# Performance work log

Measured on AMD Instinct MI355X. Metric: run time of the kernel, lower is better.

Reference implementation:

```python
import jax, jax.numpy as jnp
import numpy as np

NEG = -1e6  # mask fill value used by d2l.sequence_mask


def setup_inputs() -> dict:
    key = jax.random.key(0)
    k1, k2, k3, k4, k5, k6, k7 = jax.random.split(key, 7)
    B, Q, K, DQ, DK, H, DV = 8, 256, 1024, 256, 256, 128, 128
    queries = jax.random.normal(k1, (B, Q, DQ), dtype=jnp.float32)
    keys = jax.random.normal(k2, (B, K, DK), dtype=jnp.float32)
    values = jax.random.normal(k3, (B, K, DV), dtype=jnp.float32)
    valid_lens = jax.random.randint(k4, (B,), 1, K + 1, dtype=jnp.int32)
    # learned params (nn.Linear stores weight as [out, in]; apply as x @ W.T)
    W_q = jax.random.normal(k5, (H, DQ), dtype=jnp.float32) / np.sqrt(DQ)
    W_k = jax.random.normal(k6, (H, DK), dtype=jnp.float32) / np.sqrt(DK)
    w_v = jax.random.normal(k7, (H,), dtype=jnp.float32) / np.sqrt(H)
    return {"queries": queries, "keys": keys, "values": values,
            "valid_lens": valid_lens, "W_q": W_q, "W_k": W_k, "w_v": w_v}


def reference(queries, keys, values, valid_lens, W_q, W_k, w_v):
    # projections
    q = jnp.einsum('bqd,hd->bqh', queries, W_q)   # [B,Q,H]
    k = jnp.einsum('bkd,hd->bkh', keys, W_k)      # [B,K,H]
    # broadcast add + tanh -> [B,Q,K,H] (the fusion-headroom intermediate)
    features = jnp.tanh(q[:, :, None, :] + k[:, None, :, :])
    scores = jnp.einsum('bqkh,h->bqk', features, w_v)  # [B,Q,K]
    # masked softmax: valid_lens is per-batch (dim==1 path)
    klen = scores.shape[-1]
    mask = jnp.arange(klen)[None, None, :] < valid_lens[:, None, None]
    scores = jnp.where(mask, scores, NEG)
    weights = jax.nn.softmax(scores, axis=-1)
    # dropout is identity in eval mode
    return jnp.einsum('bqk,bkv->bqv', weights, values)
```

## Files before the change

### kernel.cpp

```cpp
#include <hip/hip_runtime.h>


#define Bb 8
#define Qn 256
#define Kk 1024
#define Dd 256
#define Hh 128
#define DVv 128

__device__ __forceinline__ float fexp2(float x) { return __builtin_amdgcn_exp2f(x); }
__device__ __forceinline__ float frcp(float x)  { return __builtin_amdgcn_rcpf(x); }

__global__ __launch_bounds__(256)
void repack_w(const float* __restrict__ Wq, const float* __restrict__ Wk,
              float4* __restrict__ Wq4T, float4* __restrict__ Wk4T)
{
    const int blk = blockIdx.x;
    const float* src = (blk < 32) ? Wq : Wk;
    float4*      dst = (blk < 32) ? Wq4T : Wk4T;
    const int idx = (blk & 31) * 256 + threadIdx.x;
    const int g = idx >> 7;
    const int h = idx & 127;
    dst[idx] = *(const float4*)(src + (size_t)h * Dd + g * 4);
}

__global__ __launch_bounds__(512)
void proj_exp_kernel(const float* __restrict__ queries,
                     const float* __restrict__ keys,
                     const float4* __restrict__ Wq4T,
                     const float4* __restrict__ Wk4T,
                     float* __restrict__ EqT,
                     float* __restrict__ EkT)
{
    __shared__ float Xs[16 * 256];
    const int blk = blockIdx.x;
    const float* X; const float4* W4; float* outT; int RB; int i0;
    if (blk < 128) { X = queries; W4 = Wq4T; outT = EqT; RB = Qn; i0 = blk * 16; }
    else           { X = keys;    W4 = Wk4T; outT = EkT; RB = Kk; i0 = (blk - 128) * 16; }
    const int tid = threadIdx.x;
    const int h   = tid & 127;
    const int r4  = __builtin_amdgcn_readfirstlane(tid >> 7);

    {
        const float4* xsrc = (const float4*)(X + (size_t)i0 * Dd);
#pragma unroll
        for (int s = 0; s < 2; ++s) {
            const int idx = tid + 512 * s;
            *(float4*)(Xs + idx * 4) = xsrc[idx];
        }
    }
    __syncthreads();

    float acc[4] = {0.f, 0.f, 0.f, 0.f};
    const float4* wp = W4 + h;
    const float*  xr = Xs + (r4 * 4) * 256;
#pragma unroll 8
    for (int g = 0; g < 64; ++g) {
        const float4 w = wp[(size_t)g * 128];
#pragma unroll
        for (int i = 0; i < 4; ++i) {
            const float4 x = *(const float4*)(xr + i * 256 + g * 4);
            acc[i] = fmaf(x.x, w.x, acc[i]);
            acc[i] = fmaf(x.y, w.y, acc[i]);
            acc[i] = fmaf(x.z, w.z, acc[i]);
            acc[i] = fmaf(x.w, w.w, acc[i]);
        }
    }
    const int b    = i0 / RB;
    const int rloc = (i0 % RB) + r4 * 4;
    float4 o;
    o.x = fexp2(acc[0] * 2.885390082f);
    o.y = fexp2(acc[1] * 2.885390082f);
    o.z = fexp2(acc[2] * 2.885390082f);
    o.w = fexp2(acc[3] * 2.885390082f);
    *(float4*)(outT + (size_t)b * Hh * RB + (size_t)h * RB + rloc) = o;
}

__global__ __launch_bounds__(256)
void score_kernel(const float* __restrict__ EqT,
                  const float* __restrict__ EkT,
                  const float* __restrict__ wv,
                  const int* __restrict__ valid_lens,
                  float* __restrict__ S)
{
    __shared__ float eqs[128 * 8];
    __shared__ float w2s[128];
    const int blk = blockIdx.x;
    const int b   = blk & 7;
    const int rem = blk >> 3;
    const int kt  = rem & 3;
    const int qt  = rem >> 2;
    const int len = valid_lens[b];
    if (kt * 256 >= len) return;

    const int tid = threadIdx.x;
    const int k   = kt * 256 + tid;
    const int q0  = qt * 8;

    {
        const int hh = tid >> 1, part = tid & 1;
        *(float4*)(eqs + hh * 8 + part * 4) =
            *(const float4*)(EqT + (size_t)b * Hh * Qn + (size_t)hh * Qn + q0 + part * 4);
        if (tid < 128) w2s[tid] = -2.0f * wv[tid];
    }
    __syncthreads();

    const float* ekp = EkT + (size_t)b * Hh * Kk + k;
    float a[8];
#pragma unroll
    for (int j = 0; j < 8; ++j) a[j] = 0.f;

#pragma unroll 4
    for (int h = 0; h < Hh; ++h) {
        const float ek = ekp[(size_t)h * Kk];
        const float w2 = w2s[h];
        const float4 e0 = *(const float4*)(eqs + h * 8);
        const float4 e1 = *(const float4*)(eqs + h * 8 + 4);
        a[0] = fmaf(w2, frcp(fmaf(e0.x, ek, 1.0f)), a[0]);
        a[1] = fmaf(w2, frcp(fmaf(e0.y, ek, 1.0f)), a[1]);
        a[2] = fmaf(w2, frcp(fmaf(e0.z, ek, 1.0f)), a[2]);
        a[3] = fmaf(w2, frcp(fmaf(e0.w, ek, 1.0f)), a[3]);
        a[4] = fmaf(w2, frcp(fmaf(e1.x, ek, 1.0f)), a[4]);
        a[5] = fmaf(w2, frcp(fmaf(e1.y, ek, 1.0f)), a[5]);
        a[6] = fmaf(w2, frcp(fmaf(e1.z, ek, 1.0f)), a[6]);
        a[7] = fmaf(w2, frcp(fmaf(e1.w, ek, 1.0f)), a[7]);
    }
    float* srow = S + (size_t)(b * Qn + q0) * Kk + k;
#pragma unroll
    for (int j = 0; j < 8; ++j) srow[(size_t)j * Kk] = a[j];
}

__global__ __launch_bounds__(512)
void softmax_pv_kernel(const float* __restrict__ S,
                       const float* __restrict__ values,
                       const int* __restrict__ valid_lens,
                       float* __restrict__ out)
{
    __shared__ float  s_sc[4][Kk];
    __shared__ float4 s_part[7][4][32];
    __shared__ float  s_inv[4];

    const int blk  = blockIdx.x;
    const int b    = blk & 7;
    const int q0   = (blk >> 3) << 2;
    const int tid  = threadIdx.x;
    const int lane = tid & 63;
    const int wave = __builtin_amdgcn_readfirstlane(tid >> 6);
    const int len  = valid_lens[b];

#pragma unroll
    for (int j = 0; j < 4; ++j) {
        const float* sr = S + (size_t)(b * Qn + q0 + j) * Kk;
        for (int k = tid; k < len; k += 512) s_sc[j][k] = sr[k];
    }
    __syncthreads();

    if (wave < 4) {
        const int q = wave;
        float m = -3.0e38f;
        for (int i = lane; i < len; i += 64) m = fmaxf(m, s_sc[q][i]);
#pragma unroll
        for (int off = 32; off > 0; off >>= 1) m = fmaxf(m, __shfl_xor(m, off));
        float sum = 0.f;
        for (int i = lane; i < len; i += 64) {
            const float p = fexp2((s_sc[q][i] - m) * 1.44269504f);
            s_sc[q][i] = p;
            sum += p;
        }
#pragma unroll
        for (int off = 32; off > 0; off >>= 1) sum += __shfl_xor(sum, off);
        if (lane == 0) s_inv[q] = frcp(sum);
    }
    __syncthreads();

    {
        const int slice = tid >> 5;
        const int l32   = tid & 31;
        const int v4    = l32 << 2;
        const float* vp = values + (size_t)b * Kk * DVv + v4;
        float a[4][4];
#pragma unroll
        for (int q = 0; q < 4; ++q) { a[q][0]=0.f; a[q][1]=0.f; a[q][2]=0.f; a[q][3]=0.f; }
        for (int k = slice; k < len; k += 16) {
            const float4 val = *(const float4*)(vp + (size_t)k * DVv);
            const float w0 = s_sc[0][k], w1 = s_sc[1][k], w2 = s_sc[2][k], w3 = s_sc[3][k];
            a[0][0] = fmaf(w0, val.x, a[0][0]);
            a[0][1] = fmaf(w0, val.y, a[0][1]);
            a[0][2] = fmaf(w0, val.z, a[0][2]);
            a[0][3] = fmaf(w0, val.w, a[0][3]);
            a[1][0] = fmaf(w1, val.x, a[1][0]);
            a[1][1] = fmaf(w1, val.y, a[1][1]);
            a[1][2] = fmaf(w1, val.z, a[1][2]);
            a[1][3] = fmaf(w1, val.w, a[1][3]);
            a[2][0] = fmaf(w2, val.x, a[2][0]);
            a[2][1] = fmaf(w2, val.y, a[2][1]);
            a[2][2] = fmaf(w2, val.z, a[2][2]);
            a[2][3] = fmaf(w2, val.w, a[2][3]);
            a[3][0] = fmaf(w3, val.x, a[3][0]);
            a[3][1] = fmaf(w3, val.y, a[3][1]);
            a[3][2] = fmaf(w3, val.z, a[3][2]);
            a[3][3] = fmaf(w3, val.w, a[3][3]);
        }
#pragma unroll
        for (int q = 0; q < 4; ++q)
#pragma unroll
            for (int x = 0; x < 4; ++x) a[q][x] += __shfl_xor(a[q][x], 32);
        if (wave > 0 && lane < 32) {
#pragma unroll
            for (int q = 0; q < 4; ++q)
                s_part[wave - 1][q][l32] = make_float4(a[q][0], a[q][1], a[q][2], a[q][3]);
        }
        __syncthreads();
        if (wave == 0 && lane < 32) {
#pragma unroll
            for (int q = 0; q < 4; ++q) {
                float r0 = a[q][0], r1 = a[q][1], r2 = a[q][2], r3 = a[q][3];
#pragma unroll
                for (int w = 0; w < 7; ++w) {
                    const float4 p = s_part[w][q][l32];
                    r0 += p.x; r1 += p.y; r2 += p.z; r3 += p.w;
                }
                const float inv = s_inv[q];
                *(float4*)(out + (size_t)(b * Qn + q0 + q) * DVv + v4) =
                    make_float4(r0 * inv, r1 * inv, r2 * inv, r3 * inv);
            }
        }
    }
}

extern "C" void kernel_launch(void* const* d_in, const int* in_sizes, int n_in,
                              void* d_out, int out_size, void* d_ws, size_t ws_size,
                              hipStream_t stream) {
    (void)in_sizes; (void)n_in; (void)out_size; (void)ws_size;
    const float* queries    = (const float*)d_in[0];
    const float* keys       = (const float*)d_in[1];
    const float* values     = (const float*)d_in[2];
    const int*   valid_lens = (const int*)  d_in[3];
    const float* Wq         = (const float*)d_in[4];
    const float* Wk         = (const float*)d_in[5];
    const float* wvv        = (const float*)d_in[6];
    float* out = (float*)d_out;

    float* Wq4T = (float*)d_ws;
    float* Wk4T = Wq4T + (size_t)Dd * Hh;
    float* EqT  = Wk4T + (size_t)Dd * Hh;
    float* EkT  = EqT + (size_t)Bb * Hh * Qn;
    float* S    = EkT + (size_t)Bb * Hh * Kk;

    repack_w       <<<  64, 256, 0, stream>>>(Wq, Wk, (float4*)Wq4T, (float4*)Wk4T);
    proj_exp_kernel<<< 640, 512, 0, stream>>>(queries, keys, (const float4*)Wq4T,
                                              (const float4*)Wk4T, EqT, EkT);
    score_kernel   <<<1024, 256, 0, stream>>>(EqT, EkT, wvv, valid_lens, S);
    softmax_pv_kernel<<<512, 512, 0, stream>>>(S, values, valid_lens, out);
}
```

Measured before the change: 145.0 us.

## Fuse score, softmax and PV into one attention kernel; retile projection through LDS

The score kernel and the softmax/PV kernel are merged into a single attn_kernel. Each block computes scores for two queries directly into LDS, so the global score matrix S is never written or re-read. The fusion uses the identity tanh(x) = 1 - 2/(1+e^{2x}), which turns the softmax max into a min over the rcp sums. The projection kernel is also retiled to 256 threads, staging W and X chunks through LDS with two h-columns per thread. In exchange, the EkT streaming over h is repeated for every query pair (eight queries per block before, two now), and each block does more serial work per query.

```diff
diff --git a/kernel.cpp b/kernel.cpp
--- a/kernel.cpp
+++ b/kernel.cpp
@@ -24,7 +24,7 @@
     dst[idx] = *(const float4*)(src + (size_t)h * Dd + g * 4);
 }
 
-__global__ __launch_bounds__(512)
+__global__ __launch_bounds__(256)
 void proj_exp_kernel(const float* __restrict__ queries,
                      const float* __restrict__ keys,
                      const float4* __restrict__ Wq4T,
@@ -32,139 +32,133 @@
                      float* __restrict__ EqT,
                      float* __restrict__ EkT)
 {
-    __shared__ float Xs[16 * 256];
+    __shared__ float Xs[16 * 64];
+    __shared__ float Ws[4][16 * 128];
+
     const int blk = blockIdx.x;
     const float* X; const float4* W4; float* outT; int RB; int i0;
     if (blk < 128) { X = queries; W4 = Wq4T; outT = EqT; RB = Qn; i0 = blk * 16; }
     else           { X = keys;    W4 = Wk4T; outT = EkT; RB = Kk; i0 = (blk - 128) * 16; }
-    const int tid = threadIdx.x;
-    const int h   = tid & 127;
-    const int r4  = __builtin_amdgcn_readfirstlane(tid >> 7);
-
-    {
-        const float4* xsrc = (const float4*)(X + (size_t)i0 * Dd);
-#pragma unroll
-        for (int s = 0; s < 2; ++s) {
-            const int idx = tid + 512 * s;
-            *(float4*)(Xs + idx * 4) = xsrc[idx];
-        }
-    }
-    __syncthreads();
-
-    float acc[4] = {0.f, 0.f, 0.f, 0.f};
-    const float4* wp = W4 + h;
-    const float*  xr = Xs + (r4 * 4) * 256;
-#pragma unroll 8
-    for (int g = 0; g < 64; ++g) {
-        const float4 w = wp[(size_t)g * 128];
-#pragma unroll
-        for (int i = 0; i < 4; ++i) {
-            const float4 x = *(const float4*)(xr + i * 256 + g * 4);
-            acc[i] = fmaf(x.x, w.x, acc[i]);
-            acc[i] = fmaf(x.y, w.y, acc[i]);
-            acc[i] = fmaf(x.z, w.z, acc[i]);
-            acc[i] = fmaf(x.w, w.w, acc[i]);
-        }
-    }
+
+    const int tid  = threadIdx.x;
+    const int hgrp = tid & 63;
+    const int rgrp = __builtin_amdgcn_readfirstlane(tid >> 6);
+    const int h0   = hgrp * 2;
+
+    float acc[4][2];
+#pragma unroll
+    for (int i = 0; i < 4; ++i) { acc[i][0] = 0.f; acc[i][1] = 0.f; }
+
+    for (int c0 = 0; c0 < Dd; c0 += 64) {
+        const int g0 = c0 >> 2;
+        __syncthreads();
+        {
+            const int row = tid >> 4, c4 = (tid & 15) * 4;
+            *(float4*)(Xs + row * 64 + c4) =
+                *(const float4*)(X + (size_t)(i0 + row) * Dd + c0 + c4);
+        }
+#pragma unroll
+        for (int s = 0; s < 8; ++s) {
+            const int idx = tid + 256 * s;
+            const int g = idx >> 7, h = idx & 127;
+            const float4 w = W4[(size_t)(g0 + g) * Hh + h];
+            Ws[0][g * 128 + h] = w.x;
+            Ws[1][g * 128 + h] = w.y;
+            Ws[2][g * 128 + h] = w.z;
+            Ws[3][g * 128 + h] = w.w;
+        }
+        __syncthreads();
+
+#pragma unroll 4
+        for (int g = 0; g < 16; ++g) {
+            float4 x[4];
+#pragma unroll
+            for (int i = 0; i < 4; ++i)
+                x[i] = *(const float4*)(Xs + (rgrp * 4 + i) * 64 + g * 4);
+#pragma unroll
+            for (int s = 0; s < 2; ++s) {
+                const int h = h0 + s;
+                const float wx = Ws[0][g * 128 + h];
+                const float wy = Ws[1][g * 128 + h];
+                const float wz = Ws[2][g * 128 + h];
+                const float ww = Ws[3][g * 128 + h];
+#pragma unroll
+                for (int i = 0; i < 4; ++i) {
+                    acc[i][s] = fmaf(x[i].x, wx, acc[i][s]);
+                    acc[i][s] = fmaf(x[i].y, wy, acc[i][s]);
+                    acc[i][s] = fmaf(x[i].z, wz, acc[i][s]);
+                    acc[i][s] = fmaf(x[i].w, ww, acc[i][s]);
+                }
+            }
+        }
+    }
+
     const int b    = i0 / RB;
-    const int rloc = (i0 % RB) + r4 * 4;
-    float4 o;
-    o.x = fexp2(acc[0] * 2.885390082f);
-    o.y = fexp2(acc[1] * 2.885390082f);
-    o.z = fexp2(acc[2] * 2.885390082f);
-    o.w = fexp2(acc[3] * 2.885390082f);
-    *(float4*)(outT + (size_t)b * Hh * RB + (size_t)h * RB + rloc) = o;
+    const int rloc = (i0 % RB) + rgrp * 4;
+#pragma unroll
+    for (int s = 0; s < 2; ++s) {
+        float4 o;
+        o.x = fexp2(acc[0][s] * 2.885390082f);
+        o.y = fexp2(acc[1][s] * 2.885390082f);
+        o.z = fexp2(acc[2][s] * 2.885390082f);
+        o.w = fexp2(acc[3][s] * 2.885390082f);
+        *(float4*)(outT + (size_t)b * Hh * RB + (size_t)(h0 + s) * RB + rloc) = o;
+    }
 }
 
 __global__ __launch_bounds__(256)
-void score_kernel(const float* __restrict__ EqT,
-                  const float* __restrict__ EkT,
-                  const float* __restrict__ wv,
-                  const int* __restrict__ valid_lens,
-                  float* __restrict__ S)
+void attn_kernel(const float* __restrict__ EqT,
+                 const float* __restrict__ EkT,
+                 const float* __restrict__ wv,
+                 const float* __restrict__ values,
+                 const int* __restrict__ valid_lens,
+                 float* __restrict__ out)
 {
-    __shared__ float eqs[128 * 8];
-    __shared__ float w2s[128];
-    const int blk = blockIdx.x;
-    const int b   = blk & 7;
-    const int rem = blk >> 3;
-    const int kt  = rem & 3;
-    const int qt  = rem >> 2;
-    const int len = valid_lens[b];
-    if (kt * 256 >= len) return;
-
-    const int tid = threadIdx.x;
-    const int k   = kt * 256 + tid;
-    const int q0  = qt * 8;
-
-    {
-        const int hh = tid >> 1, part = tid & 1;
-        *(float4*)(eqs + hh * 8 + part * 4) =
-            *(const float4*)(EqT + (size_t)b * Hh * Qn + (size_t)hh * Qn + q0 + part * 4);
-        if (tid < 128) w2s[tid] = -2.0f * wv[tid];
-    }
-    __syncthreads();
-
-    const float* ekp = EkT + (size_t)b * Hh * Kk + k;
-    float a[8];
-#pragma unroll
-    for (int j = 0; j < 8; ++j) a[j] = 0.f;
-
-#pragma unroll 4
-    for (int h = 0; h < Hh; ++h) {
-        const float ek = ekp[(size_t)h * Kk];
-        const float w2 = w2s[h];
-        const float4 e0 = *(const float4*)(eqs + h * 8);
-        const float4 e1 = *(const float4*)(eqs + h * 8 + 4);
-        a[0] = fmaf(w2, frcp(fmaf(e0.x, ek, 1.0f)), a[0]);
-        a[1] = fmaf(w2, frcp(fmaf(e0.y, ek, 1.0f)), a[1]);
-        a[2] = fmaf(w2, frcp(fmaf(e0.z, ek, 1.0f)), a[2]);
-        a[3] = fmaf(w2, frcp(fmaf(e0.w, ek, 1.0f)), a[3]);
-        a[4] = fmaf(w2, frcp(fmaf(e1.x, ek, 1.0f)), a[4]);
-        a[5] = fmaf(w2, frcp(fmaf(e1.y, ek, 1.0f)), a[5]);
-        a[6] = fmaf(w2, frcp(fmaf(e1.z, ek, 1.0f)), a[6]);
-        a[7] = fmaf(w2, frcp(fmaf(e1.w, ek, 1.0f)), a[7]);
-    }
-    float* srow = S + (size_t)(b * Qn + q0) * Kk + k;
-#pragma unroll
-    for (int j = 0; j < 8; ++j) srow[(size_t)j * Kk] = a[j];
-}
-
-__global__ __launch_bounds__(512)
-void softmax_pv_kernel(const float* __restrict__ S,
-                       const float* __restrict__ values,
-                       const int* __restrict__ valid_lens,
-                       float* __restrict__ out)
-{
-    __shared__ float  s_sc[4][Kk];
-    __shared__ float4 s_part[7][4][32];
-    __shared__ float  s_inv[4];
+    __shared__ float2 s_p[Kk];
+    __shared__ float4 s_part[3][2][32];
+    __shared__ float  s_inv[2];
 
     const int blk  = blockIdx.x;
     const int b    = blk & 7;
-    const int q0   = (blk >> 3) << 2;
+    const int q0   = (blk >> 3) * 2;
     const int tid  = threadIdx.x;
     const int lane = tid & 63;
     const int wave = __builtin_amdgcn_readfirstlane(tid >> 6);
     const int len  = valid_lens[b];
 
-#pragma unroll
-    for (int j = 0; j < 4; ++j) {
-        const float* sr = S + (size_t)(b * Qn + q0 + j) * Kk;
-        for (int k = tid; k < len; k += 512) s_sc[j][k] = sr[k];
+    const float* eqbase = EqT + (size_t)b * Hh * Qn + q0;
+    const float* ekbase = EkT + (size_t)b * Hh * Kk;
+
+    for (int k0 = 0; k0 < len; k0 += 256) {
+        const int k = k0 + tid;
+        if (k < len) {
+            const float* ekp = ekbase + k;
+            float a0 = 0.f, a1 = 0.f;
+#pragma unroll 4
+            for (int h = 0; h < Hh; ++h) {
+                const float ek = ekp[(size_t)h * Kk];
+                const float w  = wv[h];
+                const float2 eq = *(const float2*)(eqbase + (size_t)h * Qn);
+                a0 = fmaf(w, frcp(fmaf(eq.x, ek, 1.0f)), a0);
+                a1 = fmaf(w, frcp(fmaf(eq.y, ek, 1.0f)), a1);
+            }
+            s_p[k] = make_float2(a0, a1);
+        }
     }
     __syncthreads();
 
-    if (wave < 4) {
+    if (wave < 2) {
         const int q = wave;
-        float m = -3.0e38f;
-        for (int i = lane; i < len; i += 64) m = fmaxf(m, s_sc[q][i]);
-#pragma unroll
-        for (int off = 32; off > 0; off >>= 1) m = fmaxf(m, __shfl_xor(m, off));
+        const float* sp = (const float*)s_p;
+        float mn = 3.0e38f;
+        for (int i = lane; i < len; i += 64) mn = fminf(mn, sp[i * 2 + q]);
+#pragma unroll
+        for (int off = 32; off > 0; off >>= 1) mn = fminf(mn, __shfl_xor(mn, off));
         float sum = 0.f;
+        float* spw = (float*)s_p;
         for (int i = lane; i < len; i += 64) {
-            const float p = fexp2((s_sc[q][i] - m) * 1.44269504f);
-            s_sc[q][i] = p;
+            const float p = fexp2((mn - spw[i * 2 + q]) * 2.885390082f);
+            spw[i * 2 + q] = p;
             sum += p;
         }
 #pragma unroll
@@ -178,45 +172,37 @@
         const int l32   = tid & 31;
         const int v4    = l32 << 2;
         const float* vp = values + (size_t)b * Kk * DVv + v4;
-        float a[4][4];
-#pragma unroll
-        for (int q = 0; q < 4; ++q) { a[q][0]=0.f; a[q][1]=0.f; a[q][2]=0.f; a[q][3]=0.f; }
-        for (int k = slice; k < len; k += 16) {
+        float a[2][4];
+#pragma unroll
+        for (int q = 0; q < 2; ++q) { a[q][0]=0.f; a[q][1]=0.f; a[q][2]=0.f; a[q][3]=0.f; }
+        for (int k = slice; k < len; k += 8) {
             const float4 val = *(const float4*)(vp + (size_t)k * DVv);
-            const float w0 = s_sc[0][k], w1 = s_sc[1][k], w2 = s_sc[2][k], w3 = s_sc[3][k];
-            a[0][0] = fmaf(w0, val.x, a[0][0]);
-            a[0][1] = fmaf(w0, val.y, a[0][1]);
-            a[0][2] = fmaf(w0, val.z, a[0][2]);
-            a[0][3] = fmaf(w0, val.w, a[0][3]);
-            a[1][0] = fmaf(w1, val.x, a[1][0]);
-            a[1][1] = fmaf(w1, val.y, a[1][1]);
-            a[1][2] = fmaf(w1, val.z, a[1][2]);
-            a[1][3] = fmaf(w1, val.w, a[1][3]);
-            a[2][0] = fmaf(w2, val.x, a[2][0]);
-            a[2][1] = fmaf(w2, val.y, a[2][1]);
-            a[2][2] = fmaf(w2, val.z, a[2][2]);
-            a[2][3] = fmaf(w2, val.w, a[2][3]);
-            a[3][0] = fmaf(w3, val.x, a[3][0]);
-            a[3][1] = fmaf(w3, val.y, a[3][1]);
-            a[3][2] = fmaf(w3, val.z, a[3][2]);
-            a[3][3] = fmaf(w3, val.w, a[3][3]);
-        }
-#pragma unroll
-        for (int q = 0; q < 4; ++q)
+            const float2 w = s_p[k];
+            a[0][0] = fmaf(w.x, val.x, a[0][0]);
+            a[0][1] = fmaf(w.x, val.y, a[0][1]);
+            a[0][2] = fmaf(w.x, val.z, a[0][2]);
+            a[0][3] = fmaf(w.x, val.w, a[0][3]);
+            a[1][0] = fmaf(w.y, val.x, a[1][0]);
+            a[1][1] = fmaf(w.y, val.y, a[1][1]);
+            a[1][2] = fmaf(w.y, val.z, a[1][2]);
+            a[1][3] = fmaf(w.y, val.w, a[1][3]);
+        }
+#pragma unroll
+        for (int q = 0; q < 2; ++q)
 #pragma unroll
             for (int x = 0; x < 4; ++x) a[q][x] += __shfl_xor(a[q][x], 32);
         if (wave > 0 && lane < 32) {
 #pragma unroll
-            for (int q = 0; q < 4; ++q)
+            for (int q = 0; q < 2; ++q)
                 s_part[wave - 1][q][l32] = make_float4(a[q][0], a[q][1], a[q][2], a[q][3]);
         }
         __syncthreads();
         if (wave == 0 && lane < 32) {
 #pragma unroll
-            for (int q = 0; q < 4; ++q) {
+            for (int q = 0; q < 2; ++q) {
                 float r0 = a[q][0], r1 = a[q][1], r2 = a[q][2], r3 = a[q][3];
 #pragma unroll
-                for (int w = 0; w < 7; ++w) {
+                for (int w = 0; w < 3; ++w) {
                     const float4 p = s_part[w][q][l32];
                     r0 += p.x; r1 += p.y; r2 += p.z; r3 += p.w;
                 }
@@ -245,11 +231,9 @@
     float* Wk4T = Wq4T + (size_t)Dd * Hh;
     float* EqT  = Wk4T + (size_t)Dd * Hh;
     float* EkT  = EqT + (size_t)Bb * Hh * Qn;
-    float* S    = EkT + (size_t)Bb * Hh * Kk;
 
     repack_w       <<<  64, 256, 0, stream>>>(Wq, Wk, (float4*)Wq4T, (float4*)Wk4T);
-    proj_exp_kernel<<< 640, 512, 0, stream>>>(queries, keys, (const float4*)Wq4T,
+    proj_exp_kernel<<< 640, 256, 0, stream>>>(queries, keys, (const float4*)Wq4T,
                                               (const float4*)Wk4T, EqT, EkT);
-    score_kernel   <<<1024, 256, 0, stream>>>(EqT, EkT, wvv, valid_lens, S);
-    softmax_pv_kernel<<<512, 512, 0, stream>>>(S, values, valid_lens, out);
-}
+    attn_kernel    <<<1024, 256, 0, stream>>>(EqT, EkT, wvv, values, valid_lens, out);
+}
```

Measured after the change: 169.2 us. +16.7%, slower.
